# Optimization experiments

Hardware: AMD Instinct MI355X
Metric: run time of the kernel (lower is better)

The kernel has to match this reference:

```python
import jax, jax.numpy as jnp
import numpy as np

N, E = 50000, 500000
T, R, H, DK = 3, 5, 8, 16
IN = OUT = 128
SQRT_DK = float(np.sqrt(DK))
LN_EPS = 1e-5


def setup_inputs() -> dict:
    key = jax.random.key(0)
    ks = jax.random.split(key, 20)
    s = 0.05
    return {
        "x": jax.random.normal(ks[0], (N, IN), jnp.float32),
        "node_type": jax.random.randint(ks[1], (N,), 0, T),
        "src": jax.random.randint(ks[2], (E,), 0, N),
        "dst": jax.random.randint(ks[3], (E,), 0, N),
        "etype": jax.random.randint(ks[4], (E,), 0, R),
        "Wk": jax.random.normal(ks[5], (T, IN, OUT), jnp.float32) * s,
        "bk": jnp.zeros((T, OUT), jnp.float32),
        "Wq": jax.random.normal(ks[6], (T, IN, OUT), jnp.float32) * s,
        "bq": jnp.zeros((T, OUT), jnp.float32),
        "Wv": jax.random.normal(ks[7], (T, IN, OUT), jnp.float32) * s,
        "bv": jnp.zeros((T, OUT), jnp.float32),
        "Wa": jax.random.normal(ks[8], (T, OUT, OUT), jnp.float32) * s,
        "ba": jnp.zeros((T, OUT), jnp.float32),
        "rel_pri": jnp.ones((R, H), jnp.float32),
        "rel_att": jax.random.normal(ks[9], (R, H, DK, DK), jnp.float32) * s,
        "rel_msg": jax.random.normal(ks[10], (R, H, DK, DK), jnp.float32) * s,
        "skip": jnp.ones((T,), jnp.float32),
        "ln_g": jnp.ones((T, OUT), jnp.float32),
        "ln_b": jnp.zeros((T, OUT), jnp.float32),
    }


def _typed_proj(x, node_type, W, b):
    # apply all per-ntype Linears, then pick each node's own type
    y = jnp.einsum('ni,tio->nto', x, W) + b[None]            # [N,T,OUT]
    return jnp.take_along_axis(y, node_type[:, None, None], axis=1)[:, 0]


def reference(x, node_type, src, dst, etype, Wk, bk, Wq, bq, Wv, bv, Wa, ba,
              rel_pri, rel_att, rel_msg, skip, ln_g, ln_b):
    n = x.shape[0]
    k = _typed_proj(x, node_type, Wk, bk).reshape(n, H, DK)
    q = _typed_proj(x, node_type, Wq, bq).reshape(n, H, DK)
    v = _typed_proj(x, node_type, Wv, bv).reshape(n, H, DK)

    ks_e, vs_e, q_e = k[src], v[src], q[dst]                 # [E,H,DK]
    # relation-specific bmm: loop over the small fixed set of etypes
    key_e = jnp.zeros_like(ks_e)
    val_e = jnp.zeros_like(vs_e)
    for r in range(R):
        sel = (etype == r)[:, None, None].astype(x.dtype)
        key_e = key_e + sel * jnp.einsum('ehd,hdf->ehf', ks_e, rel_att[r])
        val_e = val_e + sel * jnp.einsum('ehd,hdf->ehf', vs_e, rel_msg[r])

    a = (q_e * key_e).sum(-1) * rel_pri[etype] / SQRT_DK     # [E,H]

    # segment softmax: per-(dst, etype) mailbox, matching DGL per-etype reduce
    seg = dst * R + etype
    NR = n * R
    m = jax.ops.segment_max(a, seg, num_segments=NR)         # [NR,H]
    m = jnp.where(jnp.isfinite(m), m, 0.0)
    p = jnp.exp(a - m[seg])
    denom = jax.ops.segment_sum(p, seg, num_segments=NR)
    attw = p / denom[seg]                                    # [E,H]

    h_seg = jax.ops.segment_sum(attw[..., None] * val_e, seg,
                                num_segments=NR).reshape(n, R, H, DK)
    cnt = jax.ops.segment_sum(jnp.ones((a.shape[0],), x.dtype), seg,
                              num_segments=NR).reshape(n, R)
    has = (cnt > 0).astype(x.dtype)                          # etypes with messages
    # cross_reducer='mean': average over etypes that delivered messages
    t = (h_seg * has[..., None, None]).sum(1)
    t = t / jnp.maximum(has.sum(1), 1.0)[:, None, None]
    t = t.reshape(n, OUT)

    trans = _typed_proj(t, node_type, Wa, ba)
    alpha = jax.nn.sigmoid(skip)[node_type][:, None]
    out = trans * alpha + x * (1.0 - alpha)

    # per-ntype LayerNorm (dropout is identity in eval)
    mu = out.mean(-1, keepdims=True)
    var = ((out - mu) ** 2).mean(-1, keepdims=True)
    out = (out - mu) * jax.lax.rsqrt(var + LN_EPS)
    out = out * ln_g[node_type] + ln_b[node_type]
    return out
```

## Files before the change

kernel.cpp:

```cpp
#include <hip/hip_runtime.h>
#include <math.h>

#define N_NODES 50000
#define N_EDGES 500000
#define NT 3
#define NRR 5
#define NH 8
#define DKH 16
#define DIM 128
#define NSEG (N_NODES * NRR)

__global__ void init_ints(int* __restrict__ base, long n_ints) {
  long i = (long)blockIdx.x * blockDim.x + threadIdx.x;
  long stride = (long)gridDim.x * blockDim.x;
  for (long j = i; j < n_ints; j += stride) base[j] = 0;
}

__global__ void bucket_nodes(const int* __restrict__ ntype, int* __restrict__ order,
                             int* __restrict__ bcnt) {
  __shared__ int lcnt[NT];
  __shared__ int lbase[NT];
  int tid = threadIdx.x;
  if (tid < NT) lcnt[tid] = 0;
  __syncthreads();
  int i = blockIdx.x * blockDim.x + tid;
  int t = -1, lp = 0;
  if (i < N_NODES) {
    t = ntype[i];
    lp = atomicAdd(&lcnt[t], 1);
  }
  __syncthreads();
  if (tid < NT) lbase[tid] = atomicAdd(&bcnt[tid], lcnt[tid]);
  __syncthreads();
  if (i < N_NODES) order[t * N_NODES + lbase[t] + lp] = i;
}

__global__ void hist_seg(const int* __restrict__ dst, const int* __restrict__ etype,
                         int* __restrict__ deg) {
  int i = blockIdx.x * blockDim.x + threadIdx.x;
  if (i >= N_EDGES) return;
  atomicAdd(&deg[dst[i] * NRR + etype[i]], 1);
}

__global__ void assign_seg(const int* __restrict__ deg, int* __restrict__ segstart,
                           int* __restrict__ gcursor) {
  int i = blockIdx.x * 256 + threadIdx.x;
  int lane = threadIdx.x & 63, wv = threadIdx.x >> 6;
  int d = (i < NSEG) ? deg[i] : 0;
  int s = d;
  #pragma unroll
  for (int m = 1; m < 64; m <<= 1) {
    int v = __shfl_up(s, m, 64);
    if (lane >= m) s += v;
  }
  __shared__ int wsum[4];
  __shared__ int wbase[4];
  __shared__ int blockbase;
  if (lane == 63) wsum[wv] = s;
  __syncthreads();
  if (threadIdx.x == 0) {
    int acc = 0;
    #pragma unroll
    for (int w = 0; w < 4; w++) { wbase[w] = acc; acc += wsum[w]; }
    blockbase = atomicAdd(gcursor, acc);
  }
  __syncthreads();
  if (i < NSEG) segstart[i] = blockbase + wbase[wv] + (s - d);
}

__global__ void scatter_seg(const int* __restrict__ src, const int* __restrict__ dst,
                            const int* __restrict__ etype,
                            const int* __restrict__ segstart, int* __restrict__ cursor,
                            int* __restrict__ meta) {
  int i = blockIdx.x * blockDim.x + threadIdx.x;
  if (i >= N_EDGES) return;
  int seg = dst[i] * NRR + etype[i];
  int pos = segstart[seg] + atomicAdd(&cursor[seg], 1);
  meta[pos] = src[i];
}

__launch_bounds__(256)
__global__ void kqv_gemm(const float* __restrict__ x,
                         const float* __restrict__ Wk, const float* __restrict__ bk,
                         const float* __restrict__ Wq, const float* __restrict__ bq,
                         const float* __restrict__ Wv, const float* __restrict__ bv,
                         float* __restrict__ kv, float* __restrict__ qb,
                         const int* __restrict__ order, const int* __restrict__ bcnt) {
  int t = blockIdx.y;
  int cnt = bcnt[t];
  int base = blockIdx.x * 64;
  if (base >= cnt) return;

  __shared__ float xs[64][129];
  __shared__ __align__(16) float wsl[8 * 128];
  __shared__ int nids[64];

  int tid = threadIdx.x;
  if (tid < 64) {
    int idx = base + tid;
    nids[tid] = (idx < cnt) ? order[t * N_NODES + idx] : -1;
  }
  __syncthreads();

  #pragma unroll
  for (int i = 0; i < 8; i++) {
    int idx = tid + i * 256;
    int node = idx >> 5, c4 = idx & 31;
    int nid = nids[node];
    float4 v = make_float4(0.f, 0.f, 0.f, 0.f);
    if (nid >= 0) v = *(const float4*)(x + (size_t)nid * DIM + c4 * 4);
    xs[node][c4 * 4 + 0] = v.x;
    xs[node][c4 * 4 + 1] = v.y;
    xs[node][c4 * 4 + 2] = v.z;
    xs[node][c4 * 4 + 3] = v.w;
  }

  int tx = tid & 15;
  int ty = tid >> 4;
  const float* Ws[3] = {Wk, Wv, Wq};
  const float* bs[3] = {bk, bv, bq};

  for (int m = 0; m < 3; m++) {
    const float* wbase = Ws[m] + (size_t)t * DIM * DIM;
    float4 acc[4][2];
    #pragma unroll
    for (int j = 0; j < 4; j++) {
      acc[j][0] = make_float4(0.f, 0.f, 0.f, 0.f);
      acc[j][1] = make_float4(0.f, 0.f, 0.f, 0.f);
    }

    for (int ks = 0; ks < 16; ks++) {
      __syncthreads();
      *(float4*)&wsl[tid * 4] = *(const float4*)(wbase + ks * 1024 + tid * 4);
      __syncthreads();
      #pragma unroll
      for (int kk = 0; kk < 8; kk++) {
        float4 w0 = *(const float4*)&wsl[kk * 128 + tx * 4];
        float4 w1 = *(const float4*)&wsl[kk * 128 + 64 + tx * 4];
        #pragma unroll
        for (int j = 0; j < 4; j++) {
          float xv = xs[ty * 4 + j][ks * 8 + kk];
          acc[j][0].x += xv * w0.x; acc[j][0].y += xv * w0.y;
          acc[j][0].z += xv * w0.z; acc[j][0].w += xv * w0.w;
          acc[j][1].x += xv * w1.x; acc[j][1].y += xv * w1.y;
          acc[j][1].z += xv * w1.z; acc[j][1].w += xv * w1.w;
        }
      }
    }

    float4 b0 = *(const float4*)(bs[m] + t * DIM + tx * 4);
    float4 b1 = *(const float4*)(bs[m] + t * DIM + 64 + tx * 4);
    #pragma unroll
    for (int j = 0; j < 4; j++) {
      int nid = nids[ty * 4 + j];
      if (nid < 0) continue;
      float* ob = (m == 2) ? (qb + (size_t)nid * DIM)
                           : (kv + (size_t)nid * 256 + (m == 1 ? 128 : 0));
      *(float4*)(ob + tx * 4)      = make_float4(acc[j][0].x + b0.x, acc[j][0].y + b0.y,
                                                 acc[j][0].z + b0.z, acc[j][0].w + b0.w);
      *(float4*)(ob + 64 + tx * 4) = make_float4(acc[j][1].x + b1.x, acc[j][1].y + b1.y,
                                                 acc[j][1].z + b1.z, acc[j][1].w + b1.w);
    }
  }
}

__launch_bounds__(256)
__global__ void rel_gather(const float* __restrict__ kv, const float* __restrict__ qmat,
                           const float* __restrict__ rel_att, const float* __restrict__ rel_msg,
                           const float* __restrict__ rel_pri,
                           const int* __restrict__ segstart, const int* __restrict__ deg,
                           const int* __restrict__ meta,
                           float* __restrict__ denom, float* __restrict__ hseg) {
  int r = blockIdx.y;
  int tid = threadIdx.x;

  __shared__ __align__(16) float As[8 * 260];
  __shared__ __align__(16) float Ms[8 * 260];
  {
    int idx = tid * 8;
    int hh = idx >> 8, w = idx & 255;
    const float4* ga = (const float4*)(rel_att + (size_t)r * 2048 + idx);
    *(float4*)&As[hh * 260 + w] = ga[0];
    *(float4*)&As[hh * 260 + w + 4] = ga[1];
    const float4* gm = (const float4*)(rel_msg + (size_t)r * 2048 + idx);
    *(float4*)&Ms[hh * 260 + w] = gm[0];
    *(float4*)&Ms[hh * 260 + w + 4] = gm[1];
  }
  __syncthreads();

  int g = tid >> 3;
  int c = tid & 7;
  int n = blockIdx.x * 32 + g;
  if (n >= N_NODES) return;
  int seg = n * NRR + r;
  int dg = deg[seg];
  if (dg == 0) {
    denom[(size_t)seg * NH + c] = 0.f;
    return;
  }
  int p0 = segstart[seg];
  float pri = rel_pri[r * NH + c] * 0.25f;

  const float4* qr = (const float4*)(qmat + (size_t)n * DIM + c * DKH);
  float4 q0 = qr[0], q1 = qr[1], q2 = qr[2], q3 = qr[3];

  float qa[16];
  #pragma unroll
  for (int d = 0; d < 16; d++) {
    const float* ar = &As[c * 260 + d * 16];
    float4 a0 = *(const float4*)(ar);
    float4 a1 = *(const float4*)(ar + 4);
    float4 a2 = *(const float4*)(ar + 8);
    float4 a3 = *(const float4*)(ar + 12);
    qa[d] = a0.x*q0.x + a0.y*q0.y + a0.z*q0.z + a0.w*q0.w
          + a1.x*q1.x + a1.y*q1.y + a1.z*q1.z + a1.w*q1.w
          + a2.x*q2.x + a2.y*q2.y + a2.z*q2.z + a2.w*q2.w
          + a3.x*q3.x + a3.y*q3.y + a3.z*q3.z + a3.w*q3.w;
  }

  float den = 0.f;
  float pv[16];
  #pragma unroll
  for (int d = 0; d < 16; d++) pv[d] = 0.f;

#define SCORE(k0_, k1_, k2_, k3_) \
  (k0_.x*qa[0]  + k0_.y*qa[1]  + k0_.z*qa[2]  + k0_.w*qa[3]  \
 + k1_.x*qa[4]  + k1_.y*qa[5]  + k1_.z*qa[6]  + k1_.w*qa[7]  \
 + k2_.x*qa[8]  + k2_.y*qa[9]  + k2_.z*qa[10] + k2_.w*qa[11] \
 + k3_.x*qa[12] + k3_.y*qa[13] + k3_.z*qa[14] + k3_.w*qa[15])

#define PVADD(p_, v0_, v1_, v2_, v3_) \
  pv[0]  += p_*v0_.x; pv[1]  += p_*v0_.y; pv[2]  += p_*v0_.z; pv[3]  += p_*v0_.w; \
  pv[4]  += p_*v1_.x; pv[5]  += p_*v1_.y; pv[6]  += p_*v1_.z; pv[7]  += p_*v1_.w; \
  pv[8]  += p_*v2_.x; pv[9]  += p_*v2_.y; pv[10] += p_*v2_.z; pv[11] += p_*v2_.w; \
  pv[12] += p_*v3_.x; pv[13] += p_*v3_.y; pv[14] += p_*v3_.z; pv[15] += p_*v3_.w;

  int e = 0;
  for (; e + 2 <= dg; e += 2) {
    int sn0 = meta[p0 + e], sn1 = meta[p0 + e + 1];
    const float4* r0 = (const float4*)(kv + (size_t)sn0 * 256 + c * DKH);
    const float4* r1 = (const float4*)(kv + (size_t)sn1 * 256 + c * DKH);
    float4 ka0 = r0[0], kb0 = r0[1], kc0 = r0[2], kd0 = r0[3];
    float4 va0 = r0[32], vb0 = r0[33], vc0 = r0[34], vd0 = r0[35];
    float4 ka1 = r1[0], kb1 = r1[1], kc1 = r1[2], kd1 = r1[3];
    float4 va1 = r1[32], vb1 = r1[33], vc1 = r1[34], vd1 = r1[35];
    float s0 = SCORE(ka0, kb0, kc0, kd0);
    float s1 = SCORE(ka1, kb1, kc1, kd1);
    float p0e = __expf(s0 * pri);
    float p1e = __expf(s1 * pri);
    den += p0e + p1e;
    PVADD(p0e, va0, vb0, vc0, vd0);
    PVADD(p1e, va1, vb1, vc1, vd1);
  }
  if (e < dg) {
    int sn0 = meta[p0 + e];
    const float4* r0 = (const float4*)(kv + (size_t)sn0 * 256 + c * DKH);
    float4 ka0 = r0[0], kb0 = r0[1], kc0 = r0[2], kd0 = r0[3];
    float4 va0 = r0[32], vb0 = r0[33], vc0 = r0[34], vd0 = r0[35];
    float s0 = SCORE(ka0, kb0, kc0, kd0);
    float p0e = __expf(s0 * pri);
    den += p0e;
    PVADD(p0e, va0, vb0, vc0, vd0);
  }
#undef SCORE
#undef PVADD

  float o[16];
  #pragma unroll
  for (int j = 0; j < 16; j++) o[j] = 0.f;
  #pragma unroll
  for (int d = 0; d < 16; d++) {
    const float* mr = &Ms[c * 260 + d * 16];
    float4 m0 = *(const float4*)(mr);
    float4 m1 = *(const float4*)(mr + 4);
    float4 m2 = *(const float4*)(mr + 8);
    float4 m3 = *(const float4*)(mr + 12);
    float p = pv[d];
    o[0]  += p*m0.x; o[1]  += p*m0.y; o[2]  += p*m0.z; o[3]  += p*m0.w;
    o[4]  += p*m1.x; o[5]  += p*m1.y; o[6]  += p*m1.z; o[7]  += p*m1.w;
    o[8]  += p*m2.x; o[9]  += p*m2.y; o[10] += p*m2.z; o[11] += p*m2.w;
    o[12] += p*m3.x; o[13] += p*m3.y; o[14] += p*m3.z; o[15] += p*m3.w;
  }
  float inv = 1.f / den;
  float4* hw = (float4*)(hseg + (size_t)seg * DIM + c * DKH);
  hw[0] = make_float4(o[0]*inv,  o[1]*inv,  o[2]*inv,  o[3]*inv);
  hw[1] = make_float4(o[4]*inv,  o[5]*inv,  o[6]*inv,  o[7]*inv);
  hw[2] = make_float4(o[8]*inv,  o[9]*inv,  o[10]*inv, o[11]*inv);
  hw[3] = make_float4(o[12]*inv, o[13]*inv, o[14]*inv, o[15]*inv);
  denom[(size_t)seg * NH + c] = den;
}

__launch_bounds__(256)
__global__ void wa_gemm_ln(const float* __restrict__ hseg, const float* __restrict__ denom,
                           const float* __restrict__ Wa, const float* __restrict__ ba,
                           const float* __restrict__ x, const float* __restrict__ skip,
                           const float* __restrict__ ln_g, const float* __restrict__ ln_b,
                           float* __restrict__ out,
                           const int* __restrict__ order, const int* __restrict__ bcnt) {
  int t = blockIdx.y;
  int cnt = bcnt[t];
  int base = blockIdx.x * 64;
  if (base >= cnt) return;

  __shared__ float xs[64][129];
  __shared__ __align__(16) float wsl[8 * 128];
  __shared__ int nids[64];

  int tid = threadIdx.x;
  if (tid < 64) {
    int idx = base + tid;
    nids[tid] = (idx < cnt) ? order[t * N_NODES + idx] : -1;
  }
  __syncthreads();

  #pragma unroll
  for (int i = 0; i < 8; i++) {
    int idx = tid + i * 256;
    int node = idx >> 5, c4 = idx & 31;
    int nid = nids[node];
    float4 v = make_float4(0.f, 0.f, 0.f, 0.f);
    if (nid >= 0) {
      int h = c4 >> 2;
      float cn = 0.f;
      float4 a = make_float4(0.f, 0.f, 0.f, 0.f);
      #pragma unroll
      for (int rr = 0; rr < NRR; rr++) {
        float den = denom[((size_t)nid * NRR + rr) * NH + h];
        if (den > 0.f) {
          float4 hv = *(const float4*)(hseg + ((size_t)nid * NRR + rr) * DIM + c4 * 4);
          a.x += hv.x; a.y += hv.y; a.z += hv.z; a.w += hv.w;
          cn += 1.f;
        }
      }
      float s = 1.f / fmaxf(cn, 1.f);
      v = make_float4(a.x * s, a.y * s, a.z * s, a.w * s);
    }
    xs[node][c4 * 4 + 0] = v.x;
    xs[node][c4 * 4 + 1] = v.y;
    xs[node][c4 * 4 + 2] = v.z;
    xs[node][c4 * 4 + 3] = v.w;
  }

  const float* wbase = Wa + (size_t)t * DIM * DIM;
  int tx = tid & 15;
  int ty = tid >> 4;
  float4 acc[4][2];
  #pragma unroll
  for (int j = 0; j < 4; j++) {
    acc[j][0] = make_float4(0.f, 0.f, 0.f, 0.f);
    acc[j][1] = make_float4(0.f, 0.f, 0.f, 0.f);
  }

  for (int ks = 0; ks < 16; ks++) {
    __syncthreads();
    *(float4*)&wsl[tid * 4] = *(const float4*)(wbase + ks * 1024 + tid * 4);
    __syncthreads();
    #pragma unroll
    for (int kk = 0; kk < 8; kk++) {
      float4 w0 = *(const float4*)&wsl[kk * 128 + tx * 4];
      float4 w1 = *(const float4*)&wsl[kk * 128 + 64 + tx * 4];
      #pragma unroll
      for (int j = 0; j < 4; j++) {
        float xv = xs[ty * 4 + j][ks * 8 + kk];
        acc[j][0].x += xv * w0.x; acc[j][0].y += xv * w0.y;
        acc[j][0].z += xv * w0.z; acc[j][0].w += xv * w0.w;
        acc[j][1].x += xv * w1.x; acc[j][1].y += xv * w1.y;
        acc[j][1].z += xv * w1.z; acc[j][1].w += xv * w1.w;
      }
    }
  }

  float alpha = 1.f / (1.f + __expf(-skip[t]));
  float beta = 1.f - alpha;
  float4 b0 = *(const float4*)(ba + t * DIM + tx * 4);
  float4 b1 = *(const float4*)(ba + t * DIM + 64 + tx * 4);
  float4 g0 = *(const float4*)(ln_g + t * DIM + tx * 4);
  float4 g1 = *(const float4*)(ln_g + t * DIM + 64 + tx * 4);
  float4 e0 = *(const float4*)(ln_b + t * DIM + tx * 4);
  float4 e1 = *(const float4*)(ln_b + t * DIM + 64 + tx * 4);

  #pragma unroll
  for (int j = 0; j < 4; j++) {
    int nid = nids[ty * 4 + j];
    if (nid < 0) continue;
    float4 xa = *(const float4*)(x + (size_t)nid * DIM + tx * 4);
    float4 xb = *(const float4*)(x + (size_t)nid * DIM + 64 + tx * 4);
    float o[8];
    o[0] = (acc[j][0].x + b0.x) * alpha + xa.x * beta;
    o[1] = (acc[j][0].y + b0.y) * alpha + xa.y * beta;
    o[2] = (acc[j][0].z + b0.z) * alpha + xa.z * beta;
    o[3] = (acc[j][0].w + b0.w) * alpha + xa.w * beta;
    o[4] = (acc[j][1].x + b1.x) * alpha + xb.x * beta;
    o[5] = (acc[j][1].y + b1.y) * alpha + xb.y * beta;
    o[6] = (acc[j][1].z + b1.z) * alpha + xb.z * beta;
    o[7] = (acc[j][1].w + b1.w) * alpha + xb.w * beta;
    float s = o[0]+o[1]+o[2]+o[3]+o[4]+o[5]+o[6]+o[7];
    #pragma unroll
    for (int m = 1; m <= 8; m <<= 1) s += __shfl_xor(s, m);
    float mu = s * (1.f / 128.f);
    float sq = 0.f;
    #pragma unroll
    for (int i = 0; i < 8; i++) { o[i] -= mu; sq += o[i] * o[i]; }
    #pragma unroll
    for (int m = 1; m <= 8; m <<= 1) sq += __shfl_xor(sq, m);
    float rs = rsqrtf(sq * (1.f / 128.f) + 1e-5f);
    float* ob = out + (size_t)nid * DIM;
    *(float4*)(ob + tx * 4)      = make_float4(o[0]*rs*g0.x + e0.x, o[1]*rs*g0.y + e0.y,
                                               o[2]*rs*g0.z + e0.z, o[3]*rs*g0.w + e0.w);
    *(float4*)(ob + 64 + tx * 4) = make_float4(o[4]*rs*g1.x + e1.x, o[5]*rs*g1.y + e1.y,
                                               o[6]*rs*g1.z + e1.z, o[7]*rs*g1.w + e1.w);
  }
}

extern "C" void kernel_launch(void* const* d_in, const int* in_sizes, int n_in,
                              void* d_out, int out_size, void* d_ws, size_t ws_size,
                              hipStream_t stream) {
  const float* x       = (const float*)d_in[0];
  const int*   ntype   = (const int*)  d_in[1];
  const int*   src     = (const int*)  d_in[2];
  const int*   dst     = (const int*)  d_in[3];
  const int*   etype   = (const int*)  d_in[4];
  const float* Wk      = (const float*)d_in[5];
  const float* bk      = (const float*)d_in[6];
  const float* Wq      = (const float*)d_in[7];
  const float* bq      = (const float*)d_in[8];
  const float* Wv      = (const float*)d_in[9];
  const float* bv      = (const float*)d_in[10];
  const float* Wa      = (const float*)d_in[11];
  const float* ba      = (const float*)d_in[12];
  const float* rel_pri = (const float*)d_in[13];
  const float* rel_att = (const float*)d_in[14];
  const float* rel_msg = (const float*)d_in[15];
  const float* skip    = (const float*)d_in[16];
  const float* ln_g    = (const float*)d_in[17];
  const float* ln_b    = (const float*)d_in[18];
  float* out = (float*)d_out;

  float* ws = (float*)d_ws;
  size_t o = 0;
  float* kvbuf = ws + o; o += (size_t)N_NODES * 256;
  float* qbuf  = ws + o; o += (size_t)N_NODES * DIM;
  float* hseg  = ws + o; o += (size_t)NSEG * DIM;
  float* denom = ws + o; o += (size_t)NSEG * NH;
  int* order    = (int*)(ws + o); o += (size_t)N_NODES * NT;
  int* meta     = (int*)(ws + o); o += (size_t)N_EDGES;
  int* segstart = (int*)(ws + o); o += (size_t)NSEG;
  int* deg     = (int*)(ws + o); o += (size_t)NSEG;
  int* cursor  = (int*)(ws + o); o += (size_t)NSEG;
  int* cnts    = (int*)(ws + o); o += 8;
  (void)ws_size; (void)in_sizes; (void)n_in; (void)out_size;

  long nzero_ints = (long)NSEG * 2 + 8;
  init_ints<<<512, 256, 0, stream>>>(deg, nzero_ints);

  bucket_nodes<<<(N_NODES + 255) / 256, 256, 0, stream>>>(ntype, order, cnts);
  hist_seg<<<(N_EDGES + 255) / 256, 256, 0, stream>>>(dst, etype, deg);
  assign_seg<<<(NSEG + 255) / 256, 256, 0, stream>>>(deg, segstart, cnts + 4);
  scatter_seg<<<(N_EDGES + 255) / 256, 256, 0, stream>>>(src, dst, etype, segstart,
                                                         cursor, meta);

  dim3 gg((N_NODES + 63) / 64, NT);
  kqv_gemm<<<gg, 256, 0, stream>>>(x, Wk, bk, Wq, bq, Wv, bv, kvbuf, qbuf, order, cnts);

  dim3 gr((N_NODES + 31) / 32, NRR);
  rel_gather<<<gr, 256, 0, stream>>>(kvbuf, qbuf, rel_att, rel_msg, rel_pri,
                                     segstart, deg, meta, denom, hseg);

  wa_gemm_ln<<<gg, 256, 0, stream>>>(hseg, denom, Wa, ba, x, skip, ln_g, ln_b, out,
                                     order, cnts);
}
```

Before: 422.7 us.

## Fuse cross-relation mean into rel_gather and drop per-segment hseg buffer

The relation loop moves inside the rel_gather kernel, so each thread accumulates the per-relation attention outputs and the mean over relations that delivered messages, then writes one [N,128] tensor. This removes the [N*R,128] hseg and denom intermediates and their write-then-read traffic, and simplifies the input load in wa_gemm_ln. In exchange, rel_att and rel_msg are now read from global memory (through the caches) instead of shared memory. The grid also shrinks by a factor of R, which lowers parallelism and adds per-thread serial work.

```diff
diff --git a/kernel.cpp b/kernel.cpp
--- a/kernel.cpp
+++ b/kernel.cpp
@@ -169,59 +169,45 @@
                            const float* __restrict__ rel_att, const float* __restrict__ rel_msg,
                            const float* __restrict__ rel_pri,
                            const int* __restrict__ segstart, const int* __restrict__ deg,
-                           const int* __restrict__ meta,
-                           float* __restrict__ denom, float* __restrict__ hseg) {
-  int r = blockIdx.y;
+                           const int* __restrict__ meta, float* __restrict__ tout) {
   int tid = threadIdx.x;
-
-  __shared__ __align__(16) float As[8 * 260];
-  __shared__ __align__(16) float Ms[8 * 260];
-  {
-    int idx = tid * 8;
-    int hh = idx >> 8, w = idx & 255;
-    const float4* ga = (const float4*)(rel_att + (size_t)r * 2048 + idx);
-    *(float4*)&As[hh * 260 + w] = ga[0];
-    *(float4*)&As[hh * 260 + w + 4] = ga[1];
-    const float4* gm = (const float4*)(rel_msg + (size_t)r * 2048 + idx);
-    *(float4*)&Ms[hh * 260 + w] = gm[0];
-    *(float4*)&Ms[hh * 260 + w + 4] = gm[1];
-  }
-  __syncthreads();
-
   int g = tid >> 3;
   int c = tid & 7;
   int n = blockIdx.x * 32 + g;
   if (n >= N_NODES) return;
-  int seg = n * NRR + r;
-  int dg = deg[seg];
-  if (dg == 0) {
-    denom[(size_t)seg * NH + c] = 0.f;
-    return;
-  }
-  int p0 = segstart[seg];
-  float pri = rel_pri[r * NH + c] * 0.25f;
 
   const float4* qr = (const float4*)(qmat + (size_t)n * DIM + c * DKH);
   float4 q0 = qr[0], q1 = qr[1], q2 = qr[2], q3 = qr[3];
 
-  float qa[16];
-  #pragma unroll
-  for (int d = 0; d < 16; d++) {
-    const float* ar = &As[c * 260 + d * 16];
-    float4 a0 = *(const float4*)(ar);
-    float4 a1 = *(const float4*)(ar + 4);
-    float4 a2 = *(const float4*)(ar + 8);
-    float4 a3 = *(const float4*)(ar + 12);
-    qa[d] = a0.x*q0.x + a0.y*q0.y + a0.z*q0.z + a0.w*q0.w
-          + a1.x*q1.x + a1.y*q1.y + a1.z*q1.z + a1.w*q1.w
-          + a2.x*q2.x + a2.y*q2.y + a2.z*q2.z + a2.w*q2.w
-          + a3.x*q3.x + a3.y*q3.y + a3.z*q3.z + a3.w*q3.w;
-  }
-
-  float den = 0.f;
-  float pv[16];
-  #pragma unroll
-  for (int d = 0; d < 16; d++) pv[d] = 0.f;
+  float tacc[16];
+  #pragma unroll
+  for (int j = 0; j < 16; j++) tacc[j] = 0.f;
+  float cnt = 0.f;
+
+  for (int r = 0; r < NRR; r++) {
+    int seg = n * NRR + r;
+    int dg = deg[seg];
+    if (dg == 0) continue;
+    cnt += 1.f;
+    int p0 = segstart[seg];
+    float pri = rel_pri[r * NH + c] * 0.25f;
+
+    const float* Ab = rel_att + (size_t)(r * NH + c) * 256;
+    float qa[16];
+    #pragma unroll
+    for (int d = 0; d < 16; d++) {
+      const float4* ar = (const float4*)(Ab + d * 16);
+      float4 a0 = ar[0], a1 = ar[1], a2 = ar[2], a3 = ar[3];
+      qa[d] = a0.x*q0.x + a0.y*q0.y + a0.z*q0.z + a0.w*q0.w
+            + a1.x*q1.x + a1.y*q1.y + a1.z*q1.z + a1.w*q1.w
+            + a2.x*q2.x + a2.y*q2.y + a2.z*q2.z + a2.w*q2.w
+            + a3.x*q3.x + a3.y*q3.y + a3.z*q3.z + a3.w*q3.w;
+    }
+
+    float den = 0.f;
+    float pv[16];
+    #pragma unroll
+    for (int d = 0; d < 16; d++) pv[d] = 0.f;
 
 #define SCORE(k0_, k1_, k2_, k3_) \
   (k0_.x*qa[0]  + k0_.y*qa[1]  + k0_.z*qa[2]  + k0_.w*qa[3]  \
@@ -235,63 +221,65 @@
   pv[8]  += p_*v2_.x; pv[9]  += p_*v2_.y; pv[10] += p_*v2_.z; pv[11] += p_*v2_.w; \
   pv[12] += p_*v3_.x; pv[13] += p_*v3_.y; pv[14] += p_*v3_.z; pv[15] += p_*v3_.w;
 
-  int e = 0;
-  for (; e + 2 <= dg; e += 2) {
-    int sn0 = meta[p0 + e], sn1 = meta[p0 + e + 1];
-    const float4* r0 = (const float4*)(kv + (size_t)sn0 * 256 + c * DKH);
-    const float4* r1 = (const float4*)(kv + (size_t)sn1 * 256 + c * DKH);
-    float4 ka0 = r0[0], kb0 = r0[1], kc0 = r0[2], kd0 = r0[3];
-    float4 va0 = r0[32], vb0 = r0[33], vc0 = r0[34], vd0 = r0[35];
-    float4 ka1 = r1[0], kb1 = r1[1], kc1 = r1[2], kd1 = r1[3];
-    float4 va1 = r1[32], vb1 = r1[33], vc1 = r1[34], vd1 = r1[35];
-    float s0 = SCORE(ka0, kb0, kc0, kd0);
-    float s1 = SCORE(ka1, kb1, kc1, kd1);
-    float p0e = __expf(s0 * pri);
-    float p1e = __expf(s1 * pri);
-    den += p0e + p1e;
-    PVADD(p0e, va0, vb0, vc0, vd0);
-    PVADD(p1e, va1, vb1, vc1, vd1);
-  }
-  if (e < dg) {
-    int sn0 = meta[p0 + e];
-    const float4* r0 = (const float4*)(kv + (size_t)sn0 * 256 + c * DKH);
-    float4 ka0 = r0[0], kb0 = r0[1], kc0 = r0[2], kd0 = r0[3];
-    float4 va0 = r0[32], vb0 = r0[33], vc0 = r0[34], vd0 = r0[35];
-    float s0 = SCORE(ka0, kb0, kc0, kd0);
-    float p0e = __expf(s0 * pri);
-    den += p0e;
-    PVADD(p0e, va0, vb0, vc0, vd0);
-  }
+    int e = 0;
+    for (; e + 2 <= dg; e += 2) {
+      int sn0 = meta[p0 + e], sn1 = meta[p0 + e + 1];
+      const float4* r0 = (const float4*)(kv + (size_t)sn0 * 256 + c * DKH);
+      const float4* r1 = (const float4*)(kv + (size_t)sn1 * 256 + c * DKH);
+      float4 ka0 = r0[0], kb0 = r0[1], kc0 = r0[2], kd0 = r0[3];
+      float4 va0 = r0[32], vb0 = r0[33], vc0 = r0[34], vd0 = r0[35];
+      float4 ka1 = r1[0], kb1 = r1[1], kc1 = r1[2], kd1 = r1[3];
+      float4 va1 = r1[32], vb1 = r1[33], vc1 = r1[34], vd1 = r1[35];
+      float s0 = SCORE(ka0, kb0, kc0, kd0);
+      float s1 = SCORE(ka1, kb1, kc1, kd1);
+      float p0e = __expf(s0 * pri);
+      float p1e = __expf(s1 * pri);
+      den += p0e + p1e;
+      PVADD(p0e, va0, vb0, vc0, vd0);
+      PVADD(p1e, va1, vb1, vc1, vd1);
+    }
+    if (e < dg) {
+      int sn0 = meta[p0 + e];
+      const float4* r0 = (const float4*)(kv + (size_t)sn0 * 256 + c * DKH);
+      float4 ka0 = r0[0], kb0 = r0[1], kc0 = r0[2], kd0 = r0[3];
+      float4 va0 = r0[32], vb0 = r0[33], vc0 = r0[34], vd0 = r0[35];
+      float s0 = SCORE(ka0, kb0, kc0, kd0);
+      float p0e = __expf(s0 * pri);
+      den += p0e;
+      PVADD(p0e, va0, vb0, vc0, vd0);
+    }
 #undef SCORE
 #undef PVADD
 
-  float o[16];
-  #pragma unroll
-  for (int j = 0; j < 16; j++) o[j] = 0.f;
-  #pragma unroll
-  for (int d = 0; d < 16; d++) {
-    const float* mr = &Ms[c * 260 + d * 16];
-    float4 m0 = *(const float4*)(mr);
-    float4 m1 = *(const float4*)(mr + 4);
-    float4 m2 = *(const float4*)(mr + 8);
-    float4 m3 = *(const float4*)(mr + 12);
-    float p = pv[d];
-    o[0]  += p*m0.x; o[1]  += p*m0.y; o[2]  += p*m0.z; o[3]  += p*m0.w;
-    o[4]  += p*m1.x; o[5]  += p*m1.y; o[6]  += p*m1.z; o[7]  += p*m1.w;
-    o[8]  += p*m2.x; o[9]  += p*m2.y; o[10] += p*m2.z; o[11] += p*m2.w;
-    o[12] += p*m3.x; o[13] += p*m3.y; o[14] += p*m3.z; o[15] += p*m3.w;
-  }
-  float inv = 1.f / den;
-  float4* hw = (float4*)(hseg + (size_t)seg * DIM + c * DKH);
-  hw[0] = make_float4(o[0]*inv,  o[1]*inv,  o[2]*inv,  o[3]*inv);
-  hw[1] = make_float4(o[4]*inv,  o[5]*inv,  o[6]*inv,  o[7]*inv);
-  hw[2] = make_float4(o[8]*inv,  o[9]*inv,  o[10]*inv, o[11]*inv);
-  hw[3] = make_float4(o[12]*inv, o[13]*inv, o[14]*inv, o[15]*inv);
-  denom[(size_t)seg * NH + c] = den;
+    const float* Mb = rel_msg + (size_t)(r * NH + c) * 256;
+    float o[16];
+    #pragma unroll
+    for (int j = 0; j < 16; j++) o[j] = 0.f;
+    #pragma unroll
+    for (int d = 0; d < 16; d++) {
+      const float4* mr = (const float4*)(Mb + d * 16);
+      float4 m0 = mr[0], m1 = mr[1], m2 = mr[2], m3 = mr[3];
+      float p = pv[d];
+      o[0]  += p*m0.x; o[1]  += p*m0.y; o[2]  += p*m0.z; o[3]  += p*m0.w;
+      o[4]  += p*m1.x; o[5]  += p*m1.y; o[6]  += p*m1.z; o[7]  += p*m1.w;
+      o[8]  += p*m2.x; o[9]  += p*m2.y; o[10] += p*m2.z; o[11] += p*m2.w;
+      o[12] += p*m3.x; o[13] += p*m3.y; o[14] += p*m3.z; o[15] += p*m3.w;
+    }
+    float inv = 1.f / den;
+    #pragma unroll
+    for (int j = 0; j < 16; j++) tacc[j] += o[j] * inv;
+  }
+
+  float s = 1.f / fmaxf(cnt, 1.f);
+  float4* tw = (float4*)(tout + (size_t)n * DIM + c * DKH);
+  tw[0] = make_float4(tacc[0]*s,  tacc[1]*s,  tacc[2]*s,  tacc[3]*s);
+  tw[1] = make_float4(tacc[4]*s,  tacc[5]*s,  tacc[6]*s,  tacc[7]*s);
+  tw[2] = make_float4(tacc[8]*s,  tacc[9]*s,  tacc[10]*s, tacc[11]*s);
+  tw[3] = make_float4(tacc[12]*s, tacc[13]*s, tacc[14]*s, tacc[15]*s);
 }
 
 __launch_bounds__(256)
-__global__ void wa_gemm_ln(const float* __restrict__ hseg, const float* __restrict__ denom,
+__global__ void wa_gemm_ln(const float* __restrict__ tbuf,
                            const float* __restrict__ Wa, const float* __restrict__ ba,
                            const float* __restrict__ x, const float* __restrict__ skip,
                            const float* __restrict__ ln_g, const float* __restrict__ ln_b,
@@ -319,22 +307,7 @@
     int node = idx >> 5, c4 = idx & 31;
     int nid = nids[node];
     float4 v = make_float4(0.f, 0.f, 0.f, 0.f);
-    if (nid >= 0) {
-      int h = c4 >> 2;
-      float cn = 0.f;
-      float4 a = make_float4(0.f, 0.f, 0.f, 0.f);
-      #pragma unroll
-      for (int rr = 0; rr < NRR; rr++) {
-        float den = denom[((size_t)nid * NRR + rr) * NH + h];
-        if (den > 0.f) {
-          float4 hv = *(const float4*)(hseg + ((size_t)nid * NRR + rr) * DIM + c4 * 4);
-          a.x += hv.x; a.y += hv.y; a.z += hv.z; a.w += hv.w;
-          cn += 1.f;
-        }
-      }
-      float s = 1.f / fmaxf(cn, 1.f);
-      v = make_float4(a.x * s, a.y * s, a.z * s, a.w * s);
-    }
+    if (nid >= 0) v = *(const float4*)(tbuf + (size_t)nid * DIM + c4 * 4);
     xs[node][c4 * 4 + 0] = v.x;
     xs[node][c4 * 4 + 1] = v.y;
     xs[node][c4 * 4 + 2] = v.z;
@@ -440,8 +413,7 @@
   size_t o = 0;
   float* kvbuf = ws + o; o += (size_t)N_NODES * 256;
   float* qbuf  = ws + o; o += (size_t)N_NODES * DIM;
-  float* hseg  = ws + o; o += (size_t)NSEG * DIM;
-  float* denom = ws + o; o += (size_t)NSEG * NH;
+  float* tbuf  = ws + o; o += (size_t)N_NODES * DIM;
   int* order    = (int*)(ws + o); o += (size_t)N_NODES * NT;
   int* meta     = (int*)(ws + o); o += (size_t)N_EDGES;
   int* segstart = (int*)(ws + o); o += (size_t)NSEG;
@@ -462,10 +434,9 @@
   dim3 gg((N_NODES + 63) / 64, NT);
   kqv_gemm<<<gg, 256, 0, stream>>>(x, Wk, bk, Wq, bq, Wv, bv, kvbuf, qbuf, order, cnts);
 
-  dim3 gr((N_NODES + 31) / 32, NRR);
-  rel_gather<<<gr, 256, 0, stream>>>(kvbuf, qbuf, rel_att, rel_msg, rel_pri,
-                                     segstart, deg, meta, denom, hseg);
-
-  wa_gemm_ln<<<gg, 256, 0, stream>>>(hseg, denom, Wa, ba, x, skip, ln_g, ln_b, out,
+  rel_gather<<<(N_NODES + 31) / 32, 256, 0, stream>>>(kvbuf, qbuf, rel_att, rel_msg,
+                                                      rel_pri, segstart, deg, meta, tbuf);
+
+  wa_gemm_ln<<<gg, 256, 0, stream>>>(tbuf, Wa, ba, x, skip, ln_g, ln_b, out,
                                      order, cnts);
 }
```

Result: slower. 783.1 us (+85.3%).
